# Performance work log

Measured on AMD Instinct MI355X. Metric: run time of the kernel, lower is better.

The kernel has to match this reference:

```python
import jax, jax.numpy as jnp
import numpy as np

N = 100_000   # nodes
E = 1_600_000 # message-passing edges
EA = 1_000_000 # aux edges for bilinear head
G = 512       # graphs in batch
F_IN = 16     # num_node_features (fixed in source)
H = 32        # hidden_dim (fixed in source)


def setup_inputs() -> dict:
    key = jax.random.key(0)
    ks = jax.random.split(key, 8)
    x = jax.random.normal(ks[0], (N, F_IN), jnp.float32)
    edge_index = jax.random.randint(ks[1], (2, E), 0, N, dtype=jnp.int32)
    edge_index_aux = jax.random.randint(ks[2], (2, EA), 0, N, dtype=jnp.int32)
    batch = jnp.sort(jax.random.randint(ks[3], (N,), 0, G, dtype=jnp.int32))
    W1 = jax.random.normal(ks[4], (F_IN, H), jnp.float32) / np.sqrt(F_IN)
    b1 = jnp.zeros((H,), jnp.float32)
    W2 = jax.random.normal(ks[5], (H, H), jnp.float32) / np.sqrt(H)
    b2 = jnp.zeros((H,), jnp.float32)
    Wr = jax.random.normal(ks[6], (H, 1), jnp.float32) / np.sqrt(H)
    br = jnp.zeros((1,), jnp.float32)
    Wbil = jax.random.normal(ks[7], (1, H, H), jnp.float32) / H
    bbil = jnp.zeros((1,), jnp.float32)
    return dict(x=x, edge_index=edge_index, edge_index_aux=edge_index_aux,
                batch=batch, W1=W1, b1=b1, W2=W2, b2=b2, Wr=Wr, br=br,
                Wbil=Wbil, bbil=bbil)


def gcn_conv(x, W, b, src, dst):
    # PyG GCNConv: x' = D^{-1/2}(A+I)D^{-1/2} (x W) + b, deg includes self-loop
    xw = x @ W                                                   # [N,H]
    deg = jax.ops.segment_sum(jnp.ones((src.shape[0],), x.dtype), dst,
                              num_segments=N) + 1.0              # +1 self-loop
    dinv = jax.lax.rsqrt(deg)                                    # [N]
    coef = dinv[src] * dinv[dst]                                 # [E]
    agg = jax.ops.segment_sum(xw[src] * coef[:, None], dst, num_segments=N)
    agg = agg + xw * (dinv * dinv)[:, None]                      # self-loop msg
    return agg + b


def reference(x, edge_index, edge_index_aux, batch,
              W1, b1, W2, b2, Wr, br, Wbil, bbil):
    src, dst = edge_index[0], edge_index[1]
    h = jax.nn.relu(gcn_conv(x, W1, b1, src, dst))
    h = gcn_conv(h, W2, b2, src, dst)
    # global_mean_pool over graph ids
    cnt = jax.ops.segment_sum(jnp.ones((N,), h.dtype), batch, num_segments=G)
    pooled = jax.ops.segment_sum(h, batch, num_segments=G) / jnp.maximum(cnt, 1.0)[:, None]
    reg_output = pooled @ Wr + br                                # [G,1]
    # Bilinear edge head: out_e = x1_e^T W x2_e + b
    h1 = h[edge_index_aux[0]]                                    # [EA,H]
    h2 = h[edge_index_aux[1]]                                    # [EA,H]
    edge_pred = jnp.einsum('ei,ij,ej->e', h1, Wbil[0], h2)[:, None] + bbil
    return reg_output, edge_pred
```

## Files before the change

### kernel.cpp

```cpp
#include <hip/hip_runtime.h>
#include <hip/hip_bf16.h>
#include <string.h>

typedef __hip_bfloat16 bf16;

#define FIN 16
#define H   32
#define PADW 64
#define NB  512
#define BINCAP 4096
#define NPBMAX 200
#define PSTRIDE 65
#define CHUNK 8192
#define SCAN_CHUNK 1024
#define MAXSEG 64

__device__ __forceinline__ float b2f(bf16 v) { return __bfloat162float(v); }

__device__ __forceinline__ float loadf(const void* p, size_t i, int f32) {
    return f32 ? ((const float*)p)[i] : b2f(((const bf16*)p)[i]);
}
__device__ __forceinline__ void storef(void* p, size_t i, float v, int f32) {
    if (f32) ((float*)p)[i] = v;
    else     ((bf16*)p)[i] = __float2bfloat16(v);
}

__device__ __forceinline__ unsigned pack2(float lo, float hi) {
    bf16 a = __float2bfloat16(lo), b = __float2bfloat16(hi);
    unsigned short ua, ub;
    memcpy(&ua, &a, 2); memcpy(&ub, &b, 2);
    return ((unsigned)ub << 16) | (unsigned)ua;
}
__device__ __forceinline__ float f_lo(unsigned u) {
    union { unsigned i; float f; } v; v.i = u << 16; return v.f;
}
__device__ __forceinline__ float f_hi(unsigned u) {
    union { unsigned i; float f; } v; v.i = u & 0xffff0000u; return v.f;
}

__global__ void k_detect(const void* __restrict__ x, int nelem, int* __restrict__ flag) {
    __shared__ int cnt;
    if (threadIdx.x == 0) cnt = 0;
    __syncthreads();
    int bad = 0;
    const bf16* p = (const bf16*)x;
    for (int i = threadIdx.x; i < nelem; i += blockDim.x) {
        float v = b2f(p[i]);
        float a = fabsf(v);
        if (isnan(v) || a > 1024.f || (v != 0.f && a < 1e-20f)) bad++;
    }
    atomicAdd(&cnt, bad);
    __syncthreads();
    if (threadIdx.x == 0) flag[0] = (cnt > 64) ? 1 : 0;
}

__global__ void __launch_bounds__(1024) k_p1(
        const int* __restrict__ src, const int* __restrict__ dst,
        int* __restrict__ bincur, unsigned* __restrict__ binbuf,
        int E, int npb) {
    __shared__ int hcnt[4][NB];
    __shared__ int hbase[NB];
    __shared__ int scur[NB];
    int tid = threadIdx.x;
    int grp = tid >> 8;
    int e0 = blockIdx.x * CHUNK;
    int nE = E - e0;
    if (nE > CHUNK) nE = CHUNK;
    for (int i = tid; i < 4 * NB; i += blockDim.x) ((int*)hcnt)[i] = 0;
    __syncthreads();
    for (int i = tid; i < nE; i += blockDim.x)
        atomicAdd(&hcnt[grp][dst[e0 + i] / npb], 1);
    __syncthreads();
    for (int i = tid; i < NB; i += blockDim.x) {
        int c = hcnt[0][i] + hcnt[1][i] + hcnt[2][i] + hcnt[3][i];
        hbase[i] = c ? atomicAdd(&bincur[i], c) : 0;
        scur[i] = 0;
    }
    __syncthreads();
    for (int i = tid; i < nE; i += blockDim.x) {
        int d = dst[e0 + i];
        int bin = d / npb;
        int pos = hbase[bin] + atomicAdd(&scur[bin], 1);
        if (pos < BINCAP)
            binbuf[(size_t)bin * BINCAP + pos] =
                ((unsigned)src[e0 + i] << 10) | (unsigned)(d - bin * npb);
    }
}

__global__ void __launch_bounds__(256) k_p2(
        const int* __restrict__ bincur, const unsigned* __restrict__ binbuf,
        int* __restrict__ csr, int* __restrict__ deg, float* __restrict__ dinv,
        int N, int npb) {
    __shared__ int cur[NPBMAX];
    __shared__ int psr[NPBMAX * PSTRIDE];
    int b = blockIdx.x;
    int base = b * npb;
    int nn = N - base;
    if (nn > npb) nn = npb;
    if (nn < 0) nn = 0;
    for (int i = threadIdx.x; i < nn; i += blockDim.x) cur[i] = 0;
    __syncthreads();
    int cnt = bincur[b];
    if (cnt > BINCAP) cnt = BINCAP;
    const unsigned* buf = binbuf + (size_t)b * BINCAP;
    for (int j = threadIdx.x; j < cnt; j += blockDim.x) {
        unsigned p = buf[j];
        int loc = (int)(p & 1023u);
        int s = (int)(p >> 10);
        int pos = atomicAdd(&cur[loc], 1);
        if (pos < PADW) psr[loc * PSTRIDE + pos] = s;
    }
    __syncthreads();
    int tot = nn * PADW;
    for (int idx = threadIdx.x; idx < tot; idx += blockDim.x) {
        int i = idx >> 6, p = idx & 63;
        csr[((size_t)(base + i) << 6) + p] = psr[i * PSTRIDE + p];
    }
    for (int i = threadIdx.x; i < nn; i += blockDim.x) {
        int dg = cur[i];
        deg[base + i] = dg;
        dinv[base + i] = rsqrtf((float)dg + 1.0f);
    }
}


__global__ void k_fillp(const int* __restrict__ src, const int* __restrict__ dst,
                        int* __restrict__ cursor, int* __restrict__ csr, int E) {
    int e = blockIdx.x * blockDim.x + threadIdx.x;
    if (e >= E) return;
    int d = dst[e];
    int pos = atomicAdd(&cursor[d], 1);
    if (pos < PADW) csr[((size_t)d << 6) + pos] = src[e];
}

__global__ void k_dinvi(const int* __restrict__ deg, float* __restrict__ dinv, int N) {
    int t = blockIdx.x * blockDim.x + threadIdx.x;
    if (t < N) dinv[t] = rsqrtf((float)deg[t] + 1.0f);
}

__global__ void k_gatherpb(const int* __restrict__ deg, const int* __restrict__ csr,
                           const float* __restrict__ dinv, const unsigned* __restrict__ xsb,
                           float2* __restrict__ agg, int N) {
    int t = blockIdx.x * blockDim.x + threadIdx.x;
    int d = t >> 4, j = t & 15;
    if (d >= N) return;
    int len = deg[d];
    if (len > PADW) len = PADW;
    const int* lst = csr + ((size_t)d << 6);
    unsigned u = xsb[(size_t)d * 16 + j];
    float a0 = f_lo(u), a1 = f_hi(u);
    float b0 = 0.f, b1 = 0.f;
    int k = 0;
    for (; k + 1 < len; k += 2) {
        int s0 = lst[k], s1 = lst[k + 1];
        unsigned u0 = xsb[(size_t)s0 * 16 + j];
        unsigned u1 = xsb[(size_t)s1 * 16 + j];
        a0 += f_lo(u0); a1 += f_hi(u0);
        b0 += f_lo(u1); b1 += f_hi(u1);
    }
    if (k < len) {
        unsigned u2 = xsb[(size_t)lst[k] * 16 + j];
        a0 += f_lo(u2); a1 += f_hi(u2);
    }
    float dv = dinv[d];
    agg[(size_t)d * 16 + j] = make_float2((a0 + b0) * dv, (a1 + b1) * dv);
}


__global__ void __launch_bounds__(256) k_xw1v(
        const void* __restrict__ x, const void* __restrict__ W1,
        const float* __restrict__ dinv, const int* __restrict__ flag,
        unsigned* __restrict__ xsb, int N) {
    __shared__ float sW[FIN * H];
    __shared__ float sxx[16 * 17];
    int f32 = flag[0];
    for (int i = threadIdx.x; i < FIN * H; i += blockDim.x) sW[i] = loadf(W1, i, f32);
    __syncthreads();
    int t = blockIdx.x * blockDim.x + threadIdx.x;
    int n = t >> 4, j = t & 15, g = threadIdx.x >> 4;
    if (n < N) sxx[g * 17 + j] = loadf(x, (size_t)n * FIN + j, f32);
    __syncthreads();
    if (n >= N) return;
    float dv = dinv[n];
    float s0 = 0.f, s1 = 0.f;
    const float* xp = &sxx[g * 17];
#pragma unroll
    for (int i = 0; i < FIN; i++) {
        float xv = xp[i];
        s0 += xv * sW[i * H + 2 * j];
        s1 += xv * sW[i * H + 2 * j + 1];
    }
    xsb[(size_t)n * 16 + j] = pack2(s0 * dv, s1 * dv);
}

__global__ void __launch_bounds__(256) k_h1xw2v(
        const void* __restrict__ W2, const void* __restrict__ b1,
        const float* __restrict__ dinv, const int* __restrict__ flag,
        const float2* __restrict__ aggv, unsigned* __restrict__ xsb2, int N) {
    __shared__ float sW[H * H];
    __shared__ float sb[H];
    __shared__ float shh[16 * 33];
    int f32 = flag[0];
    for (int i = threadIdx.x; i < H * H; i += blockDim.x) sW[i] = loadf(W2, i, f32);
    if (threadIdx.x < H) sb[threadIdx.x] = loadf(b1, threadIdx.x, f32);
    __syncthreads();
    int t = blockIdx.x * blockDim.x + threadIdx.x;
    int n = t >> 4, j = t & 15, g = threadIdx.x >> 4;
    if (n < N) {
        float2 a = aggv[(size_t)n * 16 + j];
        float v0 = a.x + sb[2 * j], v1 = a.y + sb[2 * j + 1];
        shh[g * 33 + 2 * j]     = v0 > 0.f ? v0 : 0.f;
        shh[g * 33 + 2 * j + 1] = v1 > 0.f ? v1 : 0.f;
    }
    __syncthreads();
    if (n >= N) return;
    float dv = dinv[n];
    float s0 = 0.f, s1 = 0.f;
    const float* hp = &shh[g * 33];
#pragma unroll
    for (int i = 0; i < H; i++) {
        float hv = hp[i];
        s0 += hv * sW[i * H + 2 * j];
        s1 += hv * sW[i * H + 2 * j + 1];
    }
    xsb2[(size_t)n * 16 + j] = pack2(s0 * dv, s1 * dv);
}

__global__ void __launch_bounds__(256) k_hb(
        const void* __restrict__ b2v, const void* __restrict__ Wbil,
        const int* __restrict__ flag, const float2* __restrict__ aggv,
        unsigned* __restrict__ hb32, unsigned* __restrict__ gb32, int N) {
    __shared__ float sW[H * H];
    __shared__ float sb[H];
    __shared__ float shh[16 * 33];
    int f32 = flag[0];
    for (int i = threadIdx.x; i < H * H; i += blockDim.x) sW[i] = loadf(Wbil, i, f32);
    if (threadIdx.x < H) sb[threadIdx.x] = loadf(b2v, threadIdx.x, f32);
    __syncthreads();
    int t = blockIdx.x * blockDim.x + threadIdx.x;
    int n = t >> 4, j = t & 15, g = threadIdx.x >> 4;
    if (n < N) {
        float2 a = aggv[(size_t)n * 16 + j];
        float v0 = a.x + sb[2 * j], v1 = a.y + sb[2 * j + 1];
        shh[g * 33 + 2 * j]     = v0;
        shh[g * 33 + 2 * j + 1] = v1;
        hb32[(size_t)n * 16 + j] = pack2(v0, v1);
    }
    __syncthreads();
    if (n >= N) return;
    float s0 = 0.f, s1 = 0.f;
    const float* hp = &shh[g * 33];
#pragma unroll
    for (int i = 0; i < H; i++) {
        float hv = hp[i];
        s0 += hv * sW[i * H + 2 * j];
        s1 += hv * sW[i * H + 2 * j + 1];
    }
    gb32[(size_t)n * 16 + j] = pack2(s0, s1);
}

__global__ void __launch_bounds__(256) k_pool(
        const void* __restrict__ b2v, const int* __restrict__ batch,
        const int* __restrict__ flag, const float* __restrict__ aggB,
        float* __restrict__ pooled, float* __restrict__ cnt, int N) {
    __shared__ float sb[H];
    __shared__ int   sg[256];
    __shared__ float spool[MAXSEG * H];
    __shared__ float scnt[MAXSEG];
    int f32 = flag[0];
    if (threadIdx.x < H) sb[threadIdx.x] = loadf(b2v, threadIdx.x, f32);
    int blk0 = blockIdx.x * blockDim.x;
    int nvalid = N - blk0;
    if (nvalid > (int)blockDim.x) nvalid = blockDim.x;
    if ((int)threadIdx.x < nvalid) sg[threadIdx.x] = batch[blk0 + threadIdx.x];
    __syncthreads();
    int g0 = sg[0];
    int nseg = sg[nvalid - 1] - g0 + 1;
    int f = threadIdx.x & 31, k = threadIdx.x >> 5;
    if (nseg <= MAXSEG) {
        for (int i = threadIdx.x; i < nseg * H; i += blockDim.x) spool[i] = 0.f;
        for (int i = threadIdx.x; i < nseg; i += blockDim.x) scnt[i] = 0.f;
        __syncthreads();
        for (int r = k; r < nvalid; r += 8) {
            float v = aggB[(size_t)(blk0 + r) * H + f] + sb[f];
            int gl = sg[r] - g0;
            atomicAdd(&spool[gl * H + f], v);
            if (f == 0) atomicAdd(&scnt[gl], 1.f);
        }
        __syncthreads();
        for (int i = threadIdx.x; i < nseg * H; i += blockDim.x)
            atomicAdd(&pooled[(size_t)(g0 + (i >> 5)) * H + (i & 31)], spool[i]);
        for (int i = threadIdx.x; i < nseg; i += blockDim.x)
            atomicAdd(&cnt[g0 + i], scnt[i]);
    } else {
        for (int r = k; r < nvalid; r += 8) {
            float v = aggB[(size_t)(blk0 + r) * H + f] + sb[f];
            atomicAdd(&pooled[(size_t)sg[r] * H + f], v);
            if (f == 0) atomicAdd(&cnt[sg[r]], 1.f);
        }
    }
}


__global__ void k_degi(const int* __restrict__ dst, int* __restrict__ deg, int E) {
    int t = blockIdx.x * blockDim.x + threadIdx.x;
    if (t < E) atomicAdd(&deg[dst[t]], 1);
}

__global__ void k_scan1(const int* __restrict__ deg, int* __restrict__ partials, int N) {
    __shared__ int sd[256];
    int base = blockIdx.x * SCAN_CHUNK + threadIdx.x * 4;
    int s = 0;
#pragma unroll
    for (int k = 0; k < 4; k++) { int i = base + k; s += (i < N) ? deg[i] : 0; }
    sd[threadIdx.x] = s;
    __syncthreads();
    for (int off = 128; off > 0; off >>= 1) {
        if (threadIdx.x < off) sd[threadIdx.x] += sd[threadIdx.x + off];
        __syncthreads();
    }
    if (threadIdx.x == 0) partials[blockIdx.x] = sd[0];
}

__global__ void k_scan2(const int* __restrict__ partials, int* __restrict__ chunk_off, int B1) {
    __shared__ int sd[256];
    int t = threadIdx.x;
    int lv[4];
    int s = 0;
#pragma unroll
    for (int k = 0; k < 4; k++) { int i = t * 4 + k; lv[k] = (i < B1) ? partials[i] : 0; s += lv[k]; }
    sd[t] = s;
    __syncthreads();
    int inc = s;
    for (int off = 1; off < 256; off <<= 1) {
        int v = (t >= off) ? sd[t - off] : 0;
        __syncthreads();
        sd[t] += v;
        __syncthreads();
    }
    int run = sd[t] - inc;
#pragma unroll
    for (int k = 0; k < 4; k++) { int i = t * 4 + k; if (i < B1) chunk_off[i] = run; run += lv[k]; }
    if (t == 255) chunk_off[B1] = run;
}

__global__ void k_scan3(const int* __restrict__ deg, const int* __restrict__ chunk_off,
                        int* __restrict__ row_ptr, int* __restrict__ cursor,
                        int N, int E) {
    __shared__ int sd[256];
    int t = threadIdx.x;
    int base = blockIdx.x * SCAN_CHUNK + t * 4;
    int lv[4];
    int s = 0;
#pragma unroll
    for (int k = 0; k < 4; k++) { int i = base + k; lv[k] = (i < N) ? deg[i] : 0; s += lv[k]; }
    sd[t] = s;
    __syncthreads();
    int inc = s;
    for (int off = 1; off < 256; off <<= 1) {
        int v = (t >= off) ? sd[t - off] : 0;
        __syncthreads();
        sd[t] += v;
        __syncthreads();
    }
    int run = chunk_off[blockIdx.x] + sd[t] - inc;
#pragma unroll
    for (int k = 0; k < 4; k++) {
        int i = base + k;
        if (i < N) { row_ptr[i] = run; cursor[i] = run; }
        run += lv[k];
    }
    if (blockIdx.x == 0 && t == 0) row_ptr[N] = E;
}

__global__ void k_fill(const int* __restrict__ src, const int* __restrict__ dst,
                       int* __restrict__ cursor, int* __restrict__ csr, int E) {
    int e = blockIdx.x * blockDim.x + threadIdx.x;
    if (e >= E) return;
    int pos = atomicAdd(&cursor[dst[e]], 1);
    csr[pos] = src[e];
}

__global__ void k_gather(const int* __restrict__ row_ptr, const int* __restrict__ csr,
                         const float* __restrict__ dinv, const float* __restrict__ xs,
                         float* __restrict__ agg, int N) {
    int t = blockIdx.x * blockDim.x + threadIdx.x;
    int d = t >> 5, f = t & 31;
    if (d >= N) return;
    int beg = row_ptr[d], end = row_ptr[d + 1];
    float acc  = xs[(size_t)d * H + f];
    float acc2 = 0.f;
    int j = beg;
    for (; j + 1 < end; j += 2) {
        int s0 = csr[j], s1 = csr[j + 1];
        acc  += xs[(size_t)s0 * H + f];
        acc2 += xs[(size_t)s1 * H + f];
    }
    if (j < end) acc += xs[(size_t)csr[j] * H + f];
    agg[(size_t)d * H + f] = (acc + acc2) * dinv[d];
}

__global__ void k_xw1n(const void* __restrict__ x, const void* __restrict__ W1,
                       const float* __restrict__ dinv, const int* __restrict__ flag,
                       float* __restrict__ xs, int N) {
    __shared__ float sW[FIN * H];
    int f32 = flag[0];
    for (int i = threadIdx.x; i < FIN * H; i += blockDim.x) sW[i] = loadf(W1, i, f32);
    __syncthreads();
    int n = blockIdx.x * blockDim.x + threadIdx.x;
    if (n >= N) return;
    float xr[FIN];
#pragma unroll
    for (int i = 0; i < FIN; i++) xr[i] = loadf(x, (size_t)n * FIN + i, f32);
    float dv = dinv[n];
#pragma unroll
    for (int f = 0; f < H; f++) {
        float s = 0.f;
#pragma unroll
        for (int i = 0; i < FIN; i++) s += xr[i] * sW[i * H + f];
        xs[(size_t)n * H + f] = s * dv;
    }
}

__global__ void k_h1xw2n(const void* __restrict__ W2, const void* __restrict__ b1,
                         const float* __restrict__ dinv, const int* __restrict__ flag,
                         const float* __restrict__ agg, float* __restrict__ xs2, int N) {
    __shared__ float sW[H * H];
    __shared__ float sb[H];
    int f32 = flag[0];
    for (int i = threadIdx.x; i < H * H; i += blockDim.x) sW[i] = loadf(W2, i, f32);
    if (threadIdx.x < H) sb[threadIdx.x] = loadf(b1, threadIdx.x, f32);
    __syncthreads();
    int n = blockIdx.x * blockDim.x + threadIdx.x;
    if (n >= N) return;
    float hr[H];
#pragma unroll
    for (int f = 0; f < H; f++) {
        float v = agg[(size_t)n * H + f] + sb[f];
        hr[f] = v > 0.f ? v : 0.f;
    }
    float dv = dinv[n];
#pragma unroll
    for (int f = 0; f < H; f++) {
        float s = 0.f;
#pragma unroll
        for (int i = 0; i < H; i++) s += hr[i] * sW[i * H + f];
        xs2[(size_t)n * H + f] = s * dv;
    }
}


__global__ void k_degf(const int* __restrict__ dst, float* __restrict__ deg, int E) {
    int t = blockIdx.x * blockDim.x + threadIdx.x;
    if (t < E) atomicAdd(&deg[dst[t]], 1.0f);
}
__global__ void k_dinvf(float* __restrict__ deg, int N) {
    int t = blockIdx.x * blockDim.x + threadIdx.x;
    if (t < N) deg[t] = rsqrtf(deg[t] + 1.0f);
}
__global__ void k_xw1o(const void* __restrict__ x, const void* __restrict__ W1,
                       const float* __restrict__ dinv, const int* __restrict__ flag,
                       float* __restrict__ xw, float* __restrict__ agg, int N) {
    __shared__ float sW[FIN * H];
    int f32 = flag[0];
    for (int i = threadIdx.x; i < FIN * H; i += blockDim.x) sW[i] = loadf(W1, i, f32);
    __syncthreads();
    int n = blockIdx.x * blockDim.x + threadIdx.x;
    if (n >= N) return;
    float xr[FIN];
#pragma unroll
    for (int i = 0; i < FIN; i++) xr[i] = loadf(x, (size_t)n * FIN + i, f32);
    float dv = dinv[n], dv2 = dv * dv;
#pragma unroll
    for (int f = 0; f < H; f++) {
        float s = 0.f;
#pragma unroll
        for (int i = 0; i < FIN; i++) s += xr[i] * sW[i * H + f];
        xw[(size_t)n * H + f]  = s;
        agg[(size_t)n * H + f] = s * dv2;
    }
}
__global__ void k_scatter(const int* __restrict__ src, const int* __restrict__ dst,
                          const float* __restrict__ dinv, const float* __restrict__ xw,
                          float* __restrict__ agg, int E) {
    int t = blockIdx.x * blockDim.x + threadIdx.x;
    int e = t >> 5, f = t & 31;
    if (e >= E) return;
    int s = src[e], d = dst[e];
    float c = dinv[s] * dinv[d];
    atomicAdd(&agg[(size_t)d * H + f], xw[(size_t)s * H + f] * c);
}
__global__ void k_h1xw2o(const void* __restrict__ W2, const void* __restrict__ b1,
                         const float* __restrict__ dinv, const int* __restrict__ flag,
                         float* __restrict__ aggio, float* __restrict__ xw2, int N) {
    __shared__ float sW[H * H];
    __shared__ float sb[H];
    int f32 = flag[0];
    for (int i = threadIdx.x; i < H * H; i += blockDim.x) sW[i] = loadf(W2, i, f32);
    if (threadIdx.x < H) sb[threadIdx.x] = loadf(b1, threadIdx.x, f32);
    __syncthreads();
    int n = blockIdx.x * blockDim.x + threadIdx.x;
    if (n >= N) return;
    float hr[H];
#pragma unroll
    for (int f = 0; f < H; f++) {
        float v = aggio[(size_t)n * H + f] + sb[f];
        hr[f] = v > 0.f ? v : 0.f;
    }
    float dv = dinv[n], dv2 = dv * dv;
#pragma unroll
    for (int f = 0; f < H; f++) {
        float s = 0.f;
#pragma unroll
        for (int i = 0; i < H; i++) s += hr[i] * sW[i * H + f];
        xw2[(size_t)n * H + f]   = s;
        aggio[(size_t)n * H + f] = s * dv2;
    }
}


__global__ void k_reg(const float* __restrict__ pooled, const float* __restrict__ cnt,
                      const void* __restrict__ Wr, const void* __restrict__ br,
                      const int* __restrict__ flag, void* __restrict__ out, int G) {
    int f32 = flag[0];
    int g = blockIdx.x * blockDim.x + threadIdx.x;
    if (g >= G) return;
    float c = cnt[g];
    c = c > 1.f ? c : 1.f;
    float s = 0.f;
#pragma unroll
    for (int i = 0; i < H; i++) s += pooled[(size_t)g * H + i] * loadf(Wr, i, f32);
    storef(out, g, s / c + loadf(br, 0, f32), f32);
}

__global__ void k_bil(const int* __restrict__ srcA, const int* __restrict__ dstA,
                      const unsigned* __restrict__ gb32, const unsigned* __restrict__ hb32,
                      const void* __restrict__ bbil, const int* __restrict__ flag,
                      void* __restrict__ out, int G, int EA) {
    int f32 = flag[0];
    int e = blockIdx.x * blockDim.x + threadIdx.x;
    if (e >= EA) return;
    int s = srcA[e], d = dstA[e];
    const uint4* gp = (const uint4*)(gb32 + (size_t)s * (H / 2));
    const uint4* hp = (const uint4*)(hb32 + (size_t)d * (H / 2));
    float acc = 0.f;
#pragma unroll
    for (int k = 0; k < 4; k++) {
        uint4 a = gp[k], b = hp[k];
        acc += f_lo(a.x) * f_lo(b.x) + f_hi(a.x) * f_hi(b.x);
        acc += f_lo(a.y) * f_lo(b.y) + f_hi(a.y) * f_hi(b.y);
        acc += f_lo(a.z) * f_lo(b.z) + f_hi(a.z) * f_hi(b.z);
        acc += f_lo(a.w) * f_lo(b.w) + f_hi(a.w) * f_hi(b.w);
    }
    storef(out, (size_t)G + e, acc + loadf(bbil, 0, f32), f32);
}

extern "C" void kernel_launch(void* const* d_in, const int* in_sizes, int n_in,
                              void* d_out, int out_size, void* d_ws, size_t ws_size,
                              hipStream_t stream) {
    const void* x     = d_in[0];
    const int*  ei    = (const int*)d_in[1];
    const int*  eia   = (const int*)d_in[2];
    const int*  batch = (const int*)d_in[3];
    const void* W1    = d_in[4];
    const void* b1    = d_in[5];
    const void* W2    = d_in[6];
    const void* b2    = d_in[7];
    const void* Wr    = d_in[8];
    const void* br    = d_in[9];
    const void* Wbil  = d_in[10];
    const void* bbil  = d_in[11];

    const int N  = in_sizes[0] / FIN;
    const int E  = in_sizes[1] / 2;
    const int EA = in_sizes[2] / 2;
    const int G  = out_size - EA;

    float* ws     = (float*)d_ws;
    int*   flag   = (int*)ws;
    float* dinv   = ws + 16;
    float* A      = dinv + N;
    float* B      = A + (size_t)N * H;
    float* pooled = B + (size_t)N * H;
    float* cnt    = pooled + (size_t)G * H;
    float* fend   = cnt + G;

    unsigned* xsb  = (unsigned*)A;
    unsigned* hb32 = (unsigned*)A;
    unsigned* gb32 = hb32 + (size_t)N * (H / 2);

    int* degA   = (int*)fend;
    int* csrA   = degA + N;
    int* bincur = csrA + (size_t)N * PADW;
    size_t needA  = (size_t)((char*)bincur - (char*)d_ws);
    size_t needA2 = (size_t)((char*)(bincur + NB) - (char*)d_ws);
    const int B1 = (N + SCAN_CHUNK - 1) / SCAN_CHUNK;
    int* deg_i     = (int*)fend;
    int* curB      = deg_i + N;
    int* row_ptr   = curB + N;
    int* chunk_off = row_ptr + N + 1;
    int* csrB      = chunk_off + B1 + 1;
    size_t needB = (size_t)((char*)(csrB + E) - (char*)d_ws);

    const int npb = (N + NB - 1) / NB;
    const bool tierA2 = (ws_size >= needA2) && (npb <= NPBMAX) && (N <= (1 << 22)) &&
                        ((size_t)NB * BINCAP <= (size_t)N * H * 2);
    const bool tierA  = !tierA2 && (ws_size >= needA);
    const bool tierB  = !tierA2 && !tierA && (ws_size >= needB) && (B1 <= 1024);

    const int* src  = ei;
    const int* dst  = ei + E;
    const int* srcA = eia;
    const int* dstA = eia + EA;

    const int TB = 256;
    hipMemsetAsync(pooled, 0, ((size_t)G * H + G) * sizeof(float), stream);
    k_detect<<<1, TB, 0, stream>>>(x, 1024, flag);

    int ggrid16 = (int)(((long)N * 16 + TB - 1) / TB);
    int ggrid32 = (int)(((long)N * 32 + TB - 1) / TB);
    int ngrid   = (N + TB - 1) / TB;
    unsigned* xsb2 = xsb;
    float2* aggv = (float2*)B;

    if (tierA2) {
        unsigned* binbuf = (unsigned*)A;
        hipMemsetAsync(bincur, 0, NB * sizeof(int), stream);
        int nblk1 = (E + CHUNK - 1) / CHUNK;
        k_p1<<<nblk1, 1024, 0, stream>>>(src, dst, bincur, binbuf, E, npb);
        k_p2<<<NB, TB, 0, stream>>>(bincur, binbuf, csrA, degA, dinv, N, npb);
        k_xw1v<<<ggrid16, TB, 0, stream>>>(x, W1, dinv, flag, xsb, N);
        k_gatherpb<<<ggrid16, TB, 0, stream>>>(degA, csrA, dinv, xsb, aggv, N);
        k_h1xw2v<<<ggrid16, TB, 0, stream>>>(W2, b1, dinv, flag, aggv, xsb2, N);
        k_gatherpb<<<ggrid16, TB, 0, stream>>>(degA, csrA, dinv, xsb2, aggv, N);
    } else if (tierA) {
        hipMemsetAsync(degA, 0, (size_t)N * sizeof(int), stream);
        k_fillp<<<(E + TB - 1) / TB, TB, 0, stream>>>(src, dst, degA, csrA, E);
        k_dinvi<<<ngrid, TB, 0, stream>>>(degA, dinv, N);
        k_xw1v<<<ggrid16, TB, 0, stream>>>(x, W1, dinv, flag, xsb, N);
        k_gatherpb<<<ggrid16, TB, 0, stream>>>(degA, csrA, dinv, xsb, aggv, N);
        k_h1xw2v<<<ggrid16, TB, 0, stream>>>(W2, b1, dinv, flag, aggv, xsb2, N);
        k_gatherpb<<<ggrid16, TB, 0, stream>>>(degA, csrA, dinv, xsb2, aggv, N);
    } else if (tierB) {
        hipMemsetAsync(deg_i, 0, (size_t)N * sizeof(int), stream);
        k_degi<<<(E + TB - 1) / TB, TB, 0, stream>>>(dst, deg_i, E);
        k_dinvi<<<ngrid, TB, 0, stream>>>(deg_i, dinv, N);
        k_scan1<<<B1, TB, 0, stream>>>(deg_i, chunk_off, N);
        k_scan2<<<1, TB, 0, stream>>>(chunk_off, chunk_off, B1);
        k_scan3<<<B1, TB, 0, stream>>>(deg_i, chunk_off, row_ptr, curB, N, E);
        k_fill<<<(E + TB - 1) / TB, TB, 0, stream>>>(src, dst, curB, csrB, E);
        k_xw1n<<<ngrid, TB, 0, stream>>>(x, W1, dinv, flag, A, N);
        k_gather<<<ggrid32, TB, 0, stream>>>(row_ptr, csrB, dinv, A, B, N);
        k_h1xw2n<<<ngrid, TB, 0, stream>>>(W2, b1, dinv, flag, B, A, N);
        k_gather<<<ggrid32, TB, 0, stream>>>(row_ptr, csrB, dinv, A, B, N);
    } else {
        hipMemsetAsync(dinv, 0, (size_t)N * sizeof(float), stream);
        k_degf<<<(E + TB - 1) / TB, TB, 0, stream>>>(dst, dinv, E);
        k_dinvf<<<ngrid, TB, 0, stream>>>(dinv, N);
        k_xw1o<<<ngrid, TB, 0, stream>>>(x, W1, dinv, flag, A, B, N);
        long tot = (long)E * 32;
        int sgrid = (int)((tot + TB - 1) / TB);
        k_scatter<<<sgrid, TB, 0, stream>>>(src, dst, dinv, A, B, E);
        k_h1xw2o<<<ngrid, TB, 0, stream>>>(W2, b1, dinv, flag, B, A, N);
        k_scatter<<<sgrid, TB, 0, stream>>>(src, dst, dinv, A, B, E);
    }

    k_pool<<<ngrid, TB, 0, stream>>>(b2, batch, flag, B, pooled, cnt, N);
    k_hb<<<ggrid16, TB, 0, stream>>>(b2, Wbil, flag, aggv, hb32, gb32, N);
    k_reg<<<(G + TB - 1) / TB, TB, 0, stream>>>(pooled, cnt, Wr, br, flag, d_out, G);
    k_bil<<<(EA + TB - 1) / TB, TB, 0, stream>>>(srcA, dstA, gb32, hb32, bbil, flag, d_out, G, EA);
}
```

Measured before the change: 291.8 us.

## Fuse init memsets into detect kernel and fold X·W1 into CSR build

Merges the pooled and bincur memsets into the flag-detection kernel, which removes two memset launches. Fuses the first-layer X·W1 projection and dinv scaling into the per-bin CSR construction kernel, so the separate k_xw1v launch goes away. Moves binbuf out of the A buffer into its own workspace region so xsb can be written while binbuf is still being read. The tradeoff is a larger workspace requirement and X·W1 being computed by only 512 blocks, one thread per node, which may parallelise less well than the old per-element kernel. Also adds zeroing of a dummy region in the other tiers.

```diff
diff --git a/kernel.cpp b/kernel.cpp
--- a/kernel.cpp
+++ b/kernel.cpp
@@ -38,7 +38,8 @@
     union { unsigned i; float f; } v; v.i = u & 0xffff0000u; return v.f;
 }
 
-__global__ void k_detect(const void* __restrict__ x, int nelem, int* __restrict__ flag) {
+__global__ void k_init(const void* __restrict__ x, int nelem, int* __restrict__ flag,
+                       float* __restrict__ pooled, int poolN, int* __restrict__ bincur) {
     __shared__ int cnt;
     if (threadIdx.x == 0) cnt = 0;
     __syncthreads();
@@ -50,9 +51,12 @@
         if (isnan(v) || a > 1024.f || (v != 0.f && a < 1e-20f)) bad++;
     }
     atomicAdd(&cnt, bad);
+    for (int i = threadIdx.x; i < poolN; i += blockDim.x) pooled[i] = 0.f;
+    for (int i = threadIdx.x; i < NB; i += blockDim.x) bincur[i] = 0;
     __syncthreads();
     if (threadIdx.x == 0) flag[0] = (cnt > 64) ? 1 : 0;
 }
+
 
 __global__ void __launch_bounds__(1024) k_p1(
         const int* __restrict__ src, const int* __restrict__ dst,
@@ -87,12 +91,17 @@
     }
 }
 
-__global__ void __launch_bounds__(256) k_p2(
+__global__ void __launch_bounds__(256) k_p2x(
         const int* __restrict__ bincur, const unsigned* __restrict__ binbuf,
+        const void* __restrict__ x, const void* __restrict__ W1,
+        const int* __restrict__ flag,
         int* __restrict__ csr, int* __restrict__ deg, float* __restrict__ dinv,
-        int N, int npb) {
+        unsigned* __restrict__ xsb, int N, int npb) {
     __shared__ int cur[NPBMAX];
     __shared__ int psr[NPBMAX * PSTRIDE];
+    __shared__ float sW[FIN * H];
+    int f32 = flag[0];
+    for (int i = threadIdx.x; i < FIN * H; i += blockDim.x) sW[i] = loadf(W1, i, f32);
     int b = blockIdx.x;
     int base = b * npb;
     int nn = N - base;
@@ -118,8 +127,23 @@
     }
     for (int i = threadIdx.x; i < nn; i += blockDim.x) {
         int dg = cur[i];
-        deg[base + i] = dg;
-        dinv[base + i] = rsqrtf((float)dg + 1.0f);
+        int n = base + i;
+        float dv = rsqrtf((float)dg + 1.0f);
+        deg[n] = dg;
+        dinv[n] = dv;
+        float xr[FIN];
+#pragma unroll
+        for (int k = 0; k < FIN; k++) xr[k] = loadf(x, (size_t)n * FIN + k, f32);
+#pragma unroll
+        for (int f2 = 0; f2 < H / 2; f2++) {
+            float s0 = 0.f, s1 = 0.f;
+#pragma unroll
+            for (int k = 0; k < FIN; k++) {
+                s0 += xr[k] * sW[k * H + 2 * f2];
+                s1 += xr[k] * sW[k * H + 2 * f2 + 1];
+            }
+            xsb[(size_t)n * (H / 2) + f2] = pack2(s0 * dv, s1 * dv);
+        }
     }
 }
 
@@ -592,8 +616,9 @@
     int* degA   = (int*)fend;
     int* csrA   = degA + N;
     int* bincur = csrA + (size_t)N * PADW;
+    unsigned* binbuf = (unsigned*)(bincur + NB);
     size_t needA  = (size_t)((char*)bincur - (char*)d_ws);
-    size_t needA2 = (size_t)((char*)(bincur + NB) - (char*)d_ws);
+    size_t needA2 = (size_t)((char*)(binbuf + (size_t)NB * BINCAP) - (char*)d_ws);
     const int B1 = (N + SCAN_CHUNK - 1) / SCAN_CHUNK;
     int* deg_i     = (int*)fend;
     int* curB      = deg_i + N;
@@ -603,8 +628,7 @@
     size_t needB = (size_t)((char*)(csrB + E) - (char*)d_ws);
 
     const int npb = (N + NB - 1) / NB;
-    const bool tierA2 = (ws_size >= needA2) && (npb <= NPBMAX) && (N <= (1 << 22)) &&
-                        ((size_t)NB * BINCAP <= (size_t)N * H * 2);
+    const bool tierA2 = (ws_size >= needA2) && (npb <= NPBMAX) && (N <= (1 << 22));
     const bool tierA  = !tierA2 && (ws_size >= needA);
     const bool tierB  = !tierA2 && !tierA && (ws_size >= needB) && (B1 <= 1024);
 
@@ -614,9 +638,6 @@
     const int* dstA = eia + EA;
 
     const int TB = 256;
-    hipMemsetAsync(pooled, 0, ((size_t)G * H + G) * sizeof(float), stream);
-    k_detect<<<1, TB, 0, stream>>>(x, 1024, flag);
-
     int ggrid16 = (int)(((long)N * 16 + TB - 1) / TB);
     int ggrid32 = (int)(((long)N * 32 + TB - 1) / TB);
     int ngrid   = (N + TB - 1) / TB;
@@ -624,16 +645,15 @@
     float2* aggv = (float2*)B;
 
     if (tierA2) {
-        unsigned* binbuf = (unsigned*)A;
-        hipMemsetAsync(bincur, 0, NB * sizeof(int), stream);
+        k_init<<<1, TB, 0, stream>>>(x, 1024, flag, pooled, G * H + G, bincur);
         int nblk1 = (E + CHUNK - 1) / CHUNK;
         k_p1<<<nblk1, 1024, 0, stream>>>(src, dst, bincur, binbuf, E, npb);
-        k_p2<<<NB, TB, 0, stream>>>(bincur, binbuf, csrA, degA, dinv, N, npb);
-        k_xw1v<<<ggrid16, TB, 0, stream>>>(x, W1, dinv, flag, xsb, N);
+        k_p2x<<<NB, TB, 0, stream>>>(bincur, binbuf, x, W1, flag, csrA, degA, dinv, xsb, N, npb);
         k_gatherpb<<<ggrid16, TB, 0, stream>>>(degA, csrA, dinv, xsb, aggv, N);
         k_h1xw2v<<<ggrid16, TB, 0, stream>>>(W2, b1, dinv, flag, aggv, xsb2, N);
         k_gatherpb<<<ggrid16, TB, 0, stream>>>(degA, csrA, dinv, xsb2, aggv, N);
     } else if (tierA) {
+        k_init<<<1, TB, 0, stream>>>(x, 1024, flag, pooled, G * H + G, bincur);
         hipMemsetAsync(degA, 0, (size_t)N * sizeof(int), stream);
         k_fillp<<<(E + TB - 1) / TB, TB, 0, stream>>>(src, dst, degA, csrA, E);
         k_dinvi<<<ngrid, TB, 0, stream>>>(degA, dinv, N);
@@ -642,6 +662,7 @@
         k_h1xw2v<<<ggrid16, TB, 0, stream>>>(W2, b1, dinv, flag, aggv, xsb2, N);
         k_gatherpb<<<ggrid16, TB, 0, stream>>>(degA, csrA, dinv, xsb2, aggv, N);
     } else if (tierB) {
+        k_init<<<1, TB, 0, stream>>>(x, 1024, flag, pooled, G * H + G, (int*)chunk_off);
         hipMemsetAsync(deg_i, 0, (size_t)N * sizeof(int), stream);
         k_degi<<<(E + TB - 1) / TB, TB, 0, stream>>>(dst, deg_i, E);
         k_dinvi<<<ngrid, TB, 0, stream>>>(deg_i, dinv, N);
@@ -654,6 +675,7 @@
         k_h1xw2n<<<ngrid, TB, 0, stream>>>(W2, b1, dinv, flag, B, A, N);
         k_gather<<<ggrid32, TB, 0, stream>>>(row_ptr, csrB, dinv, A, B, N);
     } else {
+        k_init<<<1, TB, 0, stream>>>(x, 1024, flag, pooled, G * H + G, (int*)flag + 4);
         hipMemsetAsync(dinv, 0, (size_t)N * sizeof(float), stream);
         k_degf<<<(E + TB - 1) / TB, TB, 0, stream>>>(dst, dinv, E);
         k_dinvf<<<ngrid, TB, 0, stream>>>(dinv, N);
```

Measured after the change: 302.3 us. +3.6%, slower.
